# Kernel tuning notes

Hardware: AMD Instinct MI355X
Metric: run time of the kernel (lower is better)

## Reference

```python
import jax, jax.numpy as jnp
import numpy as np
from jax import lax

B, N, M = 4, 16384, 2048
C_IN = 64
RADII = (0.2, 0.4)
KS = (32, 64)
MLPS = ((64, 64, 128), (64, 96, 128))
EPS = 1e-5


def setup_inputs() -> dict:
    key = jax.random.key(0)
    ks = jax.random.split(key, 32)
    inp = {}
    inp["xyz"] = jax.random.uniform(ks[0], (B, 3, N), jnp.float32)
    inp["feature"] = jax.random.normal(ks[1], (B, C_IN, N), jnp.float32)
    ki = 2
    for s, chans in enumerate(MLPS):
        cin = C_IN + 3  # use_xyz concatenates relative xyz
        for l, cout in enumerate(chans):
            inp[f"w{s}{l}"] = jax.random.normal(ks[ki], (cout, cin), jnp.float32) * (1.0 / np.sqrt(cin)); ki += 1
            inp[f"g{s}{l}"] = jnp.ones((cout,), jnp.float32)
            inp[f"b{s}{l}"] = jnp.zeros((cout,), jnp.float32)
            cin = cout
    return inp


def _fps(points):
    """Farthest point sampling. points [N,3] -> [M] int32 indices (starts at 0)."""
    n = points.shape[0]
    def step(carry, _):
        dists, last = carry
        d = jnp.sum((points - points[last]) ** 2, axis=-1)
        dists = jnp.minimum(dists, d)
        nxt = jnp.argmax(dists).astype(jnp.int32)
        return (dists, nxt), nxt
    init = (jnp.full((n,), 1e10, jnp.float32), jnp.int32(0))
    _, rest = lax.scan(step, init, None, length=M - 1)
    return jnp.concatenate([jnp.zeros((1,), jnp.int32), rest])


def _ball_query(xyz, new_xyz, radius, k):
    """xyz [B,3,N], new_xyz [B,3,M] -> [B,M,k] int32. First-found semantics: empty
    slots are filled with the first valid index (pointnet2 ball_query behavior)."""
    xyz = lax.stop_gradient(xyz)
    new_xyz = lax.stop_gradient(new_xyz)
    n = xyz.shape[-1]
    sq_x = jnp.sum(xyz ** 2, axis=1)          # [B,N]
    sq_c = jnp.sum(new_xyz ** 2, axis=1)      # [B,M]
    d2 = sq_c[:, :, None] + sq_x[:, None, :] - 2.0 * jnp.einsum('bdm,bdn->bmn', new_xyz, xyz)
    scores = jnp.where(d2 < radius * radius, jnp.arange(n, dtype=jnp.int32), n)
    idx = -lax.top_k(-scores, k)[0]           # k smallest indices (in order)
    first = idx[..., :1]
    idx = jnp.where(idx >= n, first, idx)
    return jnp.where(idx >= n, 0, idx)


def _group(feat, idx):
    """feat [B,C,N], idx [B,M,K] -> [B,C,M,K]"""
    return jax.vmap(lambda f, i: f[:, i])(feat, idx)


def _forward(xyz, feature, params):
    idx = jax.vmap(_fps)(jnp.transpose(lax.stop_gradient(xyz), (0, 2, 1)))  # [B,M]
    new_xyz = jnp.take_along_axis(xyz, idx[:, None, :].astype(jnp.int32), axis=2)  # [B,3,M]
    feats = []
    for s in range(len(MLPS)):
        nidx = _ball_query(xyz, new_xyz, RADII[s], KS[s])        # [B,M,K]
        gxyz = _group(xyz, nidx) - new_xyz[..., None]            # [B,3,M,K]
        x = jnp.concatenate([gxyz, _group(feature, nidx)], axis=1)  # [B,3+C,M,K]
        for l in range(len(MLPS[s])):
            w = params[f"w{s}{l}"]; g = params[f"g{s}{l}"]; b = params[f"b{s}{l}"]
            x = jnp.einsum('oc,bcmk->bomk', w, x)                # 1x1 conv
            mu = jnp.mean(x, axis=(0, 2, 3), keepdims=True)      # train-mode BN
            var = jnp.mean((x - mu) ** 2, axis=(0, 2, 3), keepdims=True)
            x = (x - mu) * lax.rsqrt(var + EPS)
            x = x * g[None, :, None, None] + b[None, :, None, None]
            x = jax.nn.relu(x)
        feats.append(jnp.max(x, axis=3))                         # max over neighbors
    return new_xyz, jnp.concatenate(feats, axis=1)               # [B,3,M], [B,256,M]


def reference(xyz, feature, w00, g00, b00, w01, g01, b01, w02, g02, b02,
              w10, g10, b10, w11, g11, b11, w12, g12, b12):
    params = dict(w00=w00, g00=g00, b00=b00, w01=w01, g01=g01, b01=b01,
                  w02=w02, g02=g02, b02=b02, w10=w10, g10=g10, b10=b10,
                  w11=w11, g11=g11, b11=b11, w12=w12, g12=g12, b12=b12)
    return _forward(xyz, feature, params)
```

## Files before the change

### kernel.cpp

```cpp
#include <hip/hip_runtime.h>
#include <cstdint>

constexpr int B_ = 4, N_ = 16384, M_ = 2048;
constexpr int COLS0 = B_ * M_ * 32;
constexpr int COLS1 = B_ * M_ * 64;

constexpr size_t OFF_NEWXYZ = 0;
constexpr size_t OFF_NIDX0  = (size_t)B_ * 3 * M_ * 4;
constexpr size_t OFF_NIDX1  = OFF_NIDX0 + (size_t)COLS0 * 4;
constexpr size_t OFF_STATS  = OFF_NIDX1 + (size_t)COLS1 * 4;
constexpr size_t STATS_VALS = 64 * 2 * 128;
constexpr size_t OFF_COEF   = OFF_STATS + 6 * STATS_VALS * 8;
constexpr size_t OFF_MNMX   = OFF_COEF + 6 * 128 * 16;
constexpr size_t MNMX_ONE   = (size_t)B_ * M_ * 128 * 4;
constexpr size_t OFF_Z      = OFF_MNMX + 4 * MNMX_ONE;
constexpr int ZSTRIDE = 96 * 64;

__global__ __launch_bounds__(512, 2) void fps_kernel(const float* __restrict__ xyz,
                                                     float* __restrict__ newxyz,
                                                     float* __restrict__ outxyz) {
#pragma clang fp contract(off)
  int b = blockIdx.x, t = threadIdx.x;
  const float* xb = xyz + (size_t)b * 3 * N_;
  float px[32], py[32], pz[32], dd[32];
#pragma unroll
  for (int i = 0; i < 32; ++i) {
    int n = t + (i << 9);
    px[i] = xb[n]; py[i] = xb[N_ + n]; pz[i] = xb[2 * N_ + n];
    dd[i] = 1e10f;
    asm volatile("" : "+v"(px[i]), "+v"(py[i]), "+v"(pz[i]));
  }
  __shared__ float s_out[3 * M_];
  __shared__ unsigned long long s_red[8];
  __shared__ int s_w;
  float fx = xb[0], fy = xb[N_], fz = xb[2 * N_];
  if (t == 0) { s_out[0] = fx; s_out[M_] = fy; s_out[2 * M_] = fz; }
  int lane = t & 63, wid = t >> 6;
  for (int s = 1; s < M_; ++s) {
    float bv = -1.f; int bi = 0;
#pragma unroll
    for (int i = 0; i < 32; ++i) {
      float dx = px[i] - fx, dy = py[i] - fy, dz = pz[i] - fz;
      float d = (dx * dx + dy * dy) + dz * dz;
      float dm = dd[i];
      if (d < dm) dm = d;
      dd[i] = dm;
      if (dm > bv) { bv = dm; bi = t + (i << 9); }
    }
    unsigned long long key =
        ((unsigned long long)__float_as_uint(bv) << 32) | (unsigned)(0xFFFFFFFFu - (unsigned)bi);
#pragma unroll
    for (int off = 1; off < 64; off <<= 1) {
      unsigned long long o = __shfl_xor(key, off);
      if (o > key) key = o;
    }
    if (lane == 0) s_red[wid] = key;
    __syncthreads();
    if (wid == 0) {
      unsigned long long k2 = (lane < 8) ? s_red[lane] : 0ull;
#pragma unroll
      for (int off = 1; off < 8; off <<= 1) {
        unsigned long long o = __shfl_xor(k2, off);
        if (o > k2) k2 = o;
      }
      if (lane == 0) s_w = (int)(0xFFFFFFFFu - (unsigned)(k2 & 0xFFFFFFFFull));
    }
    __syncthreads();
    int w = s_w;
    fx = xb[w]; fy = xb[N_ + w]; fz = xb[2 * N_ + w];
    if (t == 0) { s_out[s] = fx; s_out[M_ + s] = fy; s_out[2 * M_ + s] = fz; }
  }
  __syncthreads();
  for (int e = t; e < 3 * M_; e += 512) {
    float v = s_out[e];
    newxyz[(size_t)b * 3 * M_ + e] = v;
    outxyz[(size_t)b * 3 * M_ + e] = v;
  }
}

template <int KNB>
__global__ __launch_bounds__(256) void bq_kernel(const float* __restrict__ xyz,
                                                 const float* __restrict__ newxyz,
                                                 int* __restrict__ nidx, float r2) {
#pragma clang fp contract(off)
  int t = threadIdx.x, lane = t & 63, wq = t >> 6;
  int q = blockIdx.x * 4 + wq;
  int b = q >> 11, m = q & 2047;
  const float* xb = xyz + (size_t)b * 3 * N_;
  float cx = newxyz[((size_t)b * 3 + 0) * M_ + m];
  float cy = newxyz[((size_t)b * 3 + 1) * M_ + m];
  float cz = newxyz[((size_t)b * 3 + 2) * M_ + m];
  float sqc = (cx * cx + cy * cy) + cz * cz;
  int found = 0, first = 0;
  for (int c = 0; c < N_ / 64; ++c) {
    int n = c * 64 + lane;
    float x = xb[n], y = xb[N_ + n], z = xb[2 * N_ + n];
    float sqx = (x * x + y * y) + z * z;
    float dot = fmaf(cz, z, fmaf(cy, y, cx * x));
    float d2 = (sqc + sqx) - 2.0f * dot;
    bool in = d2 < r2;
    unsigned long long mask = __ballot(in);
    if (mask) {
      if (found == 0) first = c * 64 + (__ffsll((long long)mask) - 1);
      int pos = found + __popcll(mask & ((1ull << lane) - 1ull));
      if (in && pos < KNB) nidx[(size_t)q * KNB + pos] = n;
      found += __popcll(mask);
      if (found >= KNB) break;
    }
  }
  if (found < KNB) {
    int fill = (found == 0) ? 0 : first;
    for (int s = found + lane; s < KNB; s += 64) nidx[(size_t)q * KNB + s] = fill;
  }
}

__device__ __forceinline__ void stat_accum(float acc, int o, int cout, double* stats,
                                           int part, int lane) {
  float v1 = acc, v2 = acc * acc;
#pragma unroll
  for (int off = 1; off < 64; off <<= 1) {
    v1 += __shfl_xor(v1, off);
    v2 += __shfl_xor(v2, off);
  }
  if (lane == 0) {
    atomicAdd(stats + ((size_t)part * 2 + 0) * cout + o, (double)v1);
    atomicAdd(stats + ((size_t)part * 2 + 1) * cout + o, (double)v2);
  }
}

template <int CIN, int G>
__device__ __forceinline__ void conv_sweep(const float* __restrict__ w, int o0,
                                           const float* sx, int lane, float* acc) {
  int o0u = __builtin_amdgcn_readfirstlane(o0);
  const float* wb = w + (size_t)o0u * CIN;
#pragma unroll
  for (int k = 0; k < G; ++k) acc[k] = 0.f;
#pragma unroll 8
  for (int c = 0; c < CIN; ++c) {
    float xv = sx[c * 64 + lane];
#pragma unroll
    for (int k = 0; k < G; ++k) acc[k] += wb[(size_t)(4 * k) * CIN + c] * xv;
  }
}

template <int CIN>
__device__ __forceinline__ void stage_bn(const float* __restrict__ zr,
                                         const float4* __restrict__ coefIn,
                                         float* sx, int t) {
  const float4* zr4 = (const float4*)zr;
  float4* sx4 = (float4*)sx;
  for (int e = t; e < CIN * 16; e += 256) {
    int c = e >> 4;
    float4 v = zr4[e];
    float4 cf = coefIn[c];
    float4 r;
    r.x = fmaxf(((v.x - cf.x) * cf.y) * cf.z + cf.w, 0.f);
    r.y = fmaxf(((v.y - cf.x) * cf.y) * cf.z + cf.w, 0.f);
    r.z = fmaxf(((v.z - cf.x) * cf.y) * cf.z + cf.w, 0.f);
    r.w = fmaxf(((v.w - cf.x) * cf.y) * cf.z + cf.w, 0.f);
    sx4[e] = r;
  }
}

template <int KNB>
__global__ __launch_bounds__(256) void convL0_kernel(
    const float* __restrict__ w0, const float* __restrict__ xyz,
    const float* __restrict__ feat, const int* __restrict__ nidx,
    const float* __restrict__ newxyz, float* __restrict__ Z, double* __restrict__ stats) {
  __shared__ float sx[67 * 64];
  __shared__ int snb[64];
  int rec = blockIdx.x, t = threadIdx.x, lane = t & 63, wid = t >> 6;
  if (t < 64) snb[t] = nidx[(size_t)rec * 64 + t];
  __syncthreads();
  for (int e = t; e < 67 * 64; e += 256) {
    int c = e >> 6, l = e & 63;
    int col = rec * 64 + l;
    int b = col / (M_ * KNB);
    int rem = col - b * (M_ * KNB);
    int m = rem / KNB;
    int n = snb[l];
    float v;
    if (c < 3) v = xyz[((size_t)b * 3 + c) * N_ + n] - newxyz[((size_t)b * 3 + c) * M_ + m];
    else       v = feat[((size_t)b * 64 + (c - 3)) * N_ + n];
    sx[e] = v;
  }
  __syncthreads();
  float* zr = Z + (size_t)rec * ZSTRIDE;
  int part = rec & 63;
  float acc[8];
#pragma unroll
  for (int g = 0; g < 2; ++g) {
    int o0 = wid + 32 * g;
    conv_sweep<67, 8>(w0, o0, sx, lane, acc);
#pragma unroll
    for (int k = 0; k < 8; ++k) {
      int o = o0 + 4 * k;
      zr[o * 64 + lane] = acc[k];
      stat_accum(acc[k], o, 64, stats, part, lane);
    }
  }
}

template <int CIN, int COUT>
__global__ __launch_bounds__(256) void convMid_kernel(
    const float* __restrict__ w, const float4* __restrict__ coefIn,
    float* __restrict__ Z, double* __restrict__ stats) {
  __shared__ float sx[CIN * 64];
  int rec = blockIdx.x, t = threadIdx.x, lane = t & 63, wid = t >> 6;
  float* zr = Z + (size_t)rec * ZSTRIDE;
  stage_bn<CIN>(zr, coefIn, sx, t);
  __syncthreads();
  int part = rec & 63;
  float acc[8];
#pragma unroll
  for (int g = 0; g < COUT / 32; ++g) {
    int o0 = wid + 32 * g;
    conv_sweep<CIN, 8>(w, o0, sx, lane, acc);
#pragma unroll
    for (int k = 0; k < 8; ++k) {
      int o = o0 + 4 * k;
      zr[o * 64 + lane] = acc[k];
      stat_accum(acc[k], o, COUT, stats, part, lane);
    }
  }
}

template <int CIN, int KNB>
__global__ __launch_bounds__(256) void convLast_kernel(
    const float* __restrict__ w, const float4* __restrict__ coefIn,
    const float* __restrict__ Z, double* __restrict__ stats,
    float* __restrict__ mx, float* __restrict__ mn) {
  __shared__ float sx[CIN * 64];
  int rec = blockIdx.x, t = threadIdx.x, lane = t & 63, wid = t >> 6;
  const float* zr = Z + (size_t)rec * ZSTRIDE;
  stage_bn<CIN>(zr, coefIn, sx, t);
  __syncthreads();
  int part = rec & 63;
  float acc[8];
#pragma unroll
  for (int g = 0; g < 4; ++g) {
    int o0 = wid + 32 * g;
    conv_sweep<CIN, 8>(w, o0, sx, lane, acc);
#pragma unroll
    for (int k = 0; k < 8; ++k) {
      int o = o0 + 4 * k;
      stat_accum(acc[k], o, 128, stats, part, lane);
      float vM = acc[k], vN = acc[k];
      if (KNB == 64) {
#pragma unroll
        for (int off = 1; off < 64; off <<= 1) {
          vM = fmaxf(vM, __shfl_xor(vM, off));
          vN = fminf(vN, __shfl_xor(vN, off));
        }
        if (lane == 0) {
          mx[(size_t)o * (B_ * M_) + rec] = vM;
          mn[(size_t)o * (B_ * M_) + rec] = vN;
        }
      } else {
#pragma unroll
        for (int off = 1; off < 32; off <<= 1) {
          vM = fmaxf(vM, __shfl_xor(vM, off));
          vN = fminf(vN, __shfl_xor(vN, off));
        }
        if ((lane & 31) == 0) {
          int grp = rec * 2 + (lane >> 5);
          mx[(size_t)o * (B_ * M_) + grp] = vM;
          mn[(size_t)o * (B_ * M_) + grp] = vN;
        }
      }
    }
  }
}

__global__ __launch_bounds__(256) void pool_fin_kernel(
    const float* __restrict__ mx, const float* __restrict__ mn,
    const float4* __restrict__ coefOut, float* __restrict__ outFeats, int chBase) {
  int idx = blockIdx.x * 256 + threadIdx.x;
  int o = idx >> 13;
  int gm = idx & 8191;
  float4 cf = coefOut[o];
  float vM = mx[idx], vN = mn[idx];
  float rM = ((vM - cf.x) * cf.y) * cf.z + cf.w;
  float rN = ((vN - cf.x) * cf.y) * cf.z + cf.w;
  float z = fmaxf(fmaxf(rM, rN), 0.f);
  int b = gm >> 11, m = gm & 2047;
  outFeats[((size_t)b * 256 + chBase + o) * M_ + m] = z;
}

__global__ void coef_kernel(const double* __restrict__ stats, const float* __restrict__ g,
                            const float* __restrict__ bb, float4* __restrict__ coef,
                            int cout, double invcnt) {
  int ch = threadIdx.x;
  if (ch >= cout) return;
  double s1 = 0.0, s2 = 0.0;
  for (int p = 0; p < 64; ++p) {
    s1 += stats[((size_t)p * 2 + 0) * cout + ch];
    s2 += stats[((size_t)p * 2 + 1) * cout + ch];
  }
  double mean = s1 * invcnt;
  double var = s2 * invcnt - mean * mean;
  double rstd = 1.0 / sqrt(var + 1e-5);
  coef[ch] = make_float4((float)mean, (float)rstd, g[ch], bb[ch]);
}

extern "C" void kernel_launch(void* const* d_in, const int* in_sizes, int n_in,
                              void* d_out, int out_size, void* d_ws, size_t ws_size,
                              hipStream_t stream) {
  const float* xyz  = (const float*)d_in[0];
  const float* feat = (const float*)d_in[1];
  const float* w00 = (const float*)d_in[2],  *g00 = (const float*)d_in[3],  *b00 = (const float*)d_in[4];
  const float* w01 = (const float*)d_in[5],  *g01 = (const float*)d_in[6],  *b01 = (const float*)d_in[7];
  const float* w02 = (const float*)d_in[8],  *g02 = (const float*)d_in[9],  *b02 = (const float*)d_in[10];
  const float* w10 = (const float*)d_in[11], *g10 = (const float*)d_in[12], *b10 = (const float*)d_in[13];
  const float* w11 = (const float*)d_in[14], *g11 = (const float*)d_in[15], *b11 = (const float*)d_in[16];
  const float* w12 = (const float*)d_in[17], *g12 = (const float*)d_in[18], *b12 = (const float*)d_in[19];

  char* ws = (char*)d_ws;
  float*  newxyz = (float*)(ws + OFF_NEWXYZ);
  int*    nidx0  = (int*)(ws + OFF_NIDX0);
  int*    nidx1  = (int*)(ws + OFF_NIDX1);
  double* stats  = (double*)(ws + OFF_STATS);
  float4* coef   = (float4*)(ws + OFF_COEF);
  float*  mx0    = (float*)(ws + OFF_MNMX + 0 * MNMX_ONE);
  float*  mn0    = (float*)(ws + OFF_MNMX + 1 * MNMX_ONE);
  float*  mx1    = (float*)(ws + OFF_MNMX + 2 * MNMX_ONE);
  float*  mn1    = (float*)(ws + OFF_MNMX + 3 * MNMX_ONE);
  float*  Z      = (float*)(ws + OFF_Z);
  float* outF = (float*)d_out;
  float* outFeats = outF + (size_t)B_ * 3 * M_;

  hipMemsetAsync(ws + OFF_STATS, 0, 6 * STATS_VALS * 8, stream);
  fps_kernel<<<B_, 512, 0, stream>>>(xyz, newxyz, outF);
  bq_kernel<32><<<(B_ * M_) / 4, 256, 0, stream>>>(xyz, newxyz, nidx0, (float)(0.2 * 0.2));
  bq_kernel<64><<<(B_ * M_) / 4, 256, 0, stream>>>(xyz, newxyz, nidx1, (float)(0.4 * 0.4));

  float4* c00 = coef + 0 * 128; float4* c01 = coef + 1 * 128; float4* c02 = coef + 2 * 128;
  float4* c10 = coef + 3 * 128; float4* c11 = coef + 4 * 128; float4* c12 = coef + 5 * 128;
  double* st0 = stats + 0 * STATS_VALS; double* st1 = stats + 1 * STATS_VALS;
  double* st2 = stats + 2 * STATS_VALS; double* st3 = stats + 3 * STATS_VALS;
  double* st4 = stats + 4 * STATS_VALS; double* st5 = stats + 5 * STATS_VALS;
  int gb0 = COLS0 / 64, gb1 = COLS1 / 64;
  int gfin = (128 * B_ * M_) / 256;

  convL0_kernel<32><<<gb0, 256, 0, stream>>>(w00, xyz, feat, nidx0, newxyz, Z, st0);
  coef_kernel<<<1, 128, 0, stream>>>(st0, g00, b00, c00, 64, 1.0 / COLS0);
  convMid_kernel<64, 64><<<gb0, 256, 0, stream>>>(w01, c00, Z, st1);
  coef_kernel<<<1, 128, 0, stream>>>(st1, g01, b01, c01, 64, 1.0 / COLS0);
  convLast_kernel<64, 32><<<gb0, 256, 0, stream>>>(w02, c01, Z, st2, mx0, mn0);
  coef_kernel<<<1, 128, 0, stream>>>(st2, g02, b02, c02, 128, 1.0 / COLS0);
  pool_fin_kernel<<<gfin, 256, 0, stream>>>(mx0, mn0, c02, outFeats, 0);

  convL0_kernel<64><<<gb1, 256, 0, stream>>>(w10, xyz, feat, nidx1, newxyz, Z, st3);
  coef_kernel<<<1, 128, 0, stream>>>(st3, g10, b10, c10, 64, 1.0 / COLS1);
  convMid_kernel<64, 96><<<gb1, 256, 0, stream>>>(w11, c10, Z, st4);
  coef_kernel<<<1, 128, 0, stream>>>(st4, g11, b11, c11, 96, 1.0 / COLS1);
  convLast_kernel<96, 64><<<gb1, 256, 0, stream>>>(w12, c11, Z, st5, mx1, mn1);
  coef_kernel<<<1, 128, 0, stream>>>(st5, g12, b12, c12, 128, 1.0 / COLS1);
  pool_fin_kernel<<<gfin, 256, 0, stream>>>(mx1, mn1, c12, outFeats, 128);
}
```

Before: 4.894 ms.

## Fuse FPS, ball query and first conv into persistent producer-consumer megakernel

Merges farthest point sampling, both ball queries and scale-1 layer-0 conv into one persistent kernel. Blocks take roles: 4 run FPS and publish centroids via atomics, 48 spin-wait on sentinel-initialized centroids to run ball queries, and the rest spin on neighbor indices to build the conv input and accumulate BN statistics. The goal is to hide the long serial FPS behind ball query and conv work instead of leaving the GPU mostly idle. It depends on all 256 blocks being co-resident and on sentinel memsets, and it adds atomic polling traffic. Scale-1 layers now run before scale-0.

```diff
diff --git a/kernel.cpp b/kernel.cpp
--- a/kernel.cpp
+++ b/kernel.cpp
@@ -16,80 +16,55 @@
 constexpr size_t OFF_Z      = OFF_MNMX + 4 * MNMX_ONE;
 constexpr int ZSTRIDE = 96 * 64;
 
-__global__ __launch_bounds__(512, 2) void fps_kernel(const float* __restrict__ xyz,
-                                                     float* __restrict__ newxyz,
-                                                     float* __restrict__ outxyz) {
+__device__ __forceinline__ void stat_accum(float acc, int o, int cout, double* stats,
+                                           int part, int lane) {
+  float v1 = acc, v2 = acc * acc;
+#pragma unroll
+  for (int off = 1; off < 64; off <<= 1) {
+    v1 += __shfl_xor(v1, off);
+    v2 += __shfl_xor(v2, off);
+  }
+  if (lane == 0) {
+    atomicAdd(stats + ((size_t)part * 2 + 0) * cout + o, (double)v1);
+    atomicAdd(stats + ((size_t)part * 2 + 1) * cout + o, (double)v2);
+  }
+}
+
+template <int CIN, int G>
+__device__ __forceinline__ void conv_sweep(const float* __restrict__ w, int o0,
+                                           const float* sx, int lane, float* acc) {
+  int o0u = __builtin_amdgcn_readfirstlane(o0);
+  const float* wb = w + (size_t)o0u * CIN;
+#pragma unroll
+  for (int k = 0; k < G; ++k) acc[k] = 0.f;
+#pragma unroll 8
+  for (int c = 0; c < CIN; ++c) {
+    float xv = sx[c * 64 + lane];
+#pragma unroll
+    for (int k = 0; k < G; ++k) acc[k] += wb[(size_t)(4 * k) * CIN + c] * xv;
+  }
+}
+
+template <int CIN>
+__device__ __forceinline__ void conv_sweep8(const float* __restrict__ w, int o0,
+                                            const float* sx, int lane, float* acc) {
+  int o0u = __builtin_amdgcn_readfirstlane(o0);
+  const float* wb = w + (size_t)o0u * CIN;
+#pragma unroll
+  for (int k = 0; k < 8; ++k) acc[k] = 0.f;
+#pragma unroll 8
+  for (int c = 0; c < CIN; ++c) {
+    float xv = sx[c * 64 + lane];
+#pragma unroll
+    for (int k = 0; k < 8; ++k) acc[k] += wb[(size_t)(8 * k) * CIN + c] * xv;
+  }
+}
+
+template <int KNB>
+__device__ void bq_wave(const float* __restrict__ xyz, int* __restrict__ nidx,
+                        int q, int b, float cx, float cy, float cz, float r2, int lane) {
 #pragma clang fp contract(off)
-  int b = blockIdx.x, t = threadIdx.x;
   const float* xb = xyz + (size_t)b * 3 * N_;
-  float px[32], py[32], pz[32], dd[32];
-#pragma unroll
-  for (int i = 0; i < 32; ++i) {
-    int n = t + (i << 9);
-    px[i] = xb[n]; py[i] = xb[N_ + n]; pz[i] = xb[2 * N_ + n];
-    dd[i] = 1e10f;
-    asm volatile("" : "+v"(px[i]), "+v"(py[i]), "+v"(pz[i]));
-  }
-  __shared__ float s_out[3 * M_];
-  __shared__ unsigned long long s_red[8];
-  __shared__ int s_w;
-  float fx = xb[0], fy = xb[N_], fz = xb[2 * N_];
-  if (t == 0) { s_out[0] = fx; s_out[M_] = fy; s_out[2 * M_] = fz; }
-  int lane = t & 63, wid = t >> 6;
-  for (int s = 1; s < M_; ++s) {
-    float bv = -1.f; int bi = 0;
-#pragma unroll
-    for (int i = 0; i < 32; ++i) {
-      float dx = px[i] - fx, dy = py[i] - fy, dz = pz[i] - fz;
-      float d = (dx * dx + dy * dy) + dz * dz;
-      float dm = dd[i];
-      if (d < dm) dm = d;
-      dd[i] = dm;
-      if (dm > bv) { bv = dm; bi = t + (i << 9); }
-    }
-    unsigned long long key =
-        ((unsigned long long)__float_as_uint(bv) << 32) | (unsigned)(0xFFFFFFFFu - (unsigned)bi);
-#pragma unroll
-    for (int off = 1; off < 64; off <<= 1) {
-      unsigned long long o = __shfl_xor(key, off);
-      if (o > key) key = o;
-    }
-    if (lane == 0) s_red[wid] = key;
-    __syncthreads();
-    if (wid == 0) {
-      unsigned long long k2 = (lane < 8) ? s_red[lane] : 0ull;
-#pragma unroll
-      for (int off = 1; off < 8; off <<= 1) {
-        unsigned long long o = __shfl_xor(k2, off);
-        if (o > k2) k2 = o;
-      }
-      if (lane == 0) s_w = (int)(0xFFFFFFFFu - (unsigned)(k2 & 0xFFFFFFFFull));
-    }
-    __syncthreads();
-    int w = s_w;
-    fx = xb[w]; fy = xb[N_ + w]; fz = xb[2 * N_ + w];
-    if (t == 0) { s_out[s] = fx; s_out[M_ + s] = fy; s_out[2 * M_ + s] = fz; }
-  }
-  __syncthreads();
-  for (int e = t; e < 3 * M_; e += 512) {
-    float v = s_out[e];
-    newxyz[(size_t)b * 3 * M_ + e] = v;
-    outxyz[(size_t)b * 3 * M_ + e] = v;
-  }
-}
-
-template <int KNB>
-__global__ __launch_bounds__(256) void bq_kernel(const float* __restrict__ xyz,
-                                                 const float* __restrict__ newxyz,
-                                                 int* __restrict__ nidx, float r2) {
-#pragma clang fp contract(off)
-  int t = threadIdx.x, lane = t & 63, wq = t >> 6;
-  int q = blockIdx.x * 4 + wq;
-  int b = q >> 11, m = q & 2047;
-  const float* xb = xyz + (size_t)b * 3 * N_;
-  float cx = newxyz[((size_t)b * 3 + 0) * M_ + m];
-  float cy = newxyz[((size_t)b * 3 + 1) * M_ + m];
-  float cz = newxyz[((size_t)b * 3 + 2) * M_ + m];
   float sqc = (cx * cx + cy * cy) + cz * cz;
   int found = 0, first = 0;
   for (int c = 0; c < N_ / 64; ++c) {
@@ -103,43 +78,150 @@
     if (mask) {
       if (found == 0) first = c * 64 + (__ffsll((long long)mask) - 1);
       int pos = found + __popcll(mask & ((1ull << lane) - 1ull));
-      if (in && pos < KNB) nidx[(size_t)q * KNB + pos] = n;
+      if (in && pos < KNB) atomicExch(&nidx[(size_t)q * KNB + pos], n);
       found += __popcll(mask);
       if (found >= KNB) break;
     }
   }
   if (found < KNB) {
     int fill = (found == 0) ? 0 : first;
-    for (int s = found + lane; s < KNB; s += 64) nidx[(size_t)q * KNB + s] = fill;
-  }
-}
-
-__device__ __forceinline__ void stat_accum(float acc, int o, int cout, double* stats,
-                                           int part, int lane) {
-  float v1 = acc, v2 = acc * acc;
-#pragma unroll
-  for (int off = 1; off < 64; off <<= 1) {
-    v1 += __shfl_xor(v1, off);
-    v2 += __shfl_xor(v2, off);
-  }
-  if (lane == 0) {
-    atomicAdd(stats + ((size_t)part * 2 + 0) * cout + o, (double)v1);
-    atomicAdd(stats + ((size_t)part * 2 + 1) * cout + o, (double)v2);
-  }
-}
-
-template <int CIN, int G>
-__device__ __forceinline__ void conv_sweep(const float* __restrict__ w, int o0,
-                                           const float* sx, int lane, float* acc) {
-  int o0u = __builtin_amdgcn_readfirstlane(o0);
-  const float* wb = w + (size_t)o0u * CIN;
-#pragma unroll
-  for (int k = 0; k < G; ++k) acc[k] = 0.f;
-#pragma unroll 8
-  for (int c = 0; c < CIN; ++c) {
-    float xv = sx[c * 64 + lane];
-#pragma unroll
-    for (int k = 0; k < G; ++k) acc[k] += wb[(size_t)(4 * k) * CIN + c] * xv;
+    for (int s2 = found + lane; s2 < KNB; s2 += 64) atomicExch(&nidx[(size_t)q * KNB + s2], fill);
+  }
+}
+
+__global__ __launch_bounds__(512, 2) void mega_kernel(
+    const float* __restrict__ xyz, const float* __restrict__ feat,
+    float* __restrict__ newxyz, float* __restrict__ outxyz,
+    int* __restrict__ nidx0, int* __restrict__ nidx1,
+    float* __restrict__ Z, double* __restrict__ st3, const float* __restrict__ w10) {
+  __shared__ __align__(16) char smem[98304];
+  int bid = blockIdx.x, t = threadIdx.x, lane = t & 63, wid = t >> 6;
+
+  if (bid < 4) {
+#pragma clang fp contract(off)
+    float* s_out = (float*)smem;
+    unsigned long long* s_red = (unsigned long long*)(smem + 24576);
+    int* s_w = (int*)(smem + 24640);
+    int b = bid;
+    const float* xb = xyz + (size_t)b * 3 * N_;
+    float px[32], py[32], pz[32], dd[32];
+#pragma unroll
+    for (int i = 0; i < 32; ++i) {
+      int n = t + (i << 9);
+      px[i] = xb[n]; py[i] = xb[N_ + n]; pz[i] = xb[2 * N_ + n];
+      dd[i] = 1e10f;
+      asm volatile("" : "+v"(px[i]), "+v"(py[i]), "+v"(pz[i]));
+    }
+    size_t base = (size_t)b * 3 * M_;
+    float fx = xb[0], fy = xb[N_], fz = xb[2 * N_];
+    if (t == 0) {
+      s_out[0] = fx; s_out[M_] = fy; s_out[2 * M_] = fz;
+      atomicExch(&newxyz[base], fx); atomicExch(&newxyz[base + M_], fy);
+      atomicExch(&newxyz[base + 2 * M_], fz);
+    }
+    for (int s = 1; s < M_; ++s) {
+      float bv = -1.f; int bi = 0;
+#pragma unroll
+      for (int i = 0; i < 32; ++i) {
+        float dx = px[i] - fx, dy = py[i] - fy, dz = pz[i] - fz;
+        float d = (dx * dx + dy * dy) + dz * dz;
+        float dm = dd[i];
+        if (d < dm) dm = d;
+        dd[i] = dm;
+        if (dm > bv) { bv = dm; bi = t + (i << 9); }
+      }
+      unsigned long long key =
+          ((unsigned long long)__float_as_uint(bv) << 32) | (unsigned)(0xFFFFFFFFu - (unsigned)bi);
+#pragma unroll
+      for (int off = 1; off < 64; off <<= 1) {
+        unsigned long long o = __shfl_xor(key, off);
+        if (o > key) key = o;
+      }
+      if (lane == 0) s_red[wid] = key;
+      __syncthreads();
+      if (wid == 0) {
+        unsigned long long k2 = (lane < 8) ? s_red[lane] : 0ull;
+#pragma unroll
+        for (int off = 1; off < 8; off <<= 1) {
+          unsigned long long o = __shfl_xor(k2, off);
+          if (o > k2) k2 = o;
+        }
+        if (lane == 0) *s_w = (int)(0xFFFFFFFFu - (unsigned)(k2 & 0xFFFFFFFFull));
+      }
+      __syncthreads();
+      int w = *s_w;
+      fx = xb[w]; fy = xb[N_ + w]; fz = xb[2 * N_ + w];
+      if (t == 0) {
+        s_out[s] = fx; s_out[M_ + s] = fy; s_out[2 * M_ + s] = fz;
+        atomicExch(&newxyz[base + s], fx); atomicExch(&newxyz[base + M_ + s], fy);
+        atomicExch(&newxyz[base + 2 * M_ + s], fz);
+      }
+    }
+    __syncthreads();
+    for (int e = t; e < 3 * M_; e += 512) outxyz[base + e] = s_out[e];
+  } else if (bid < 52) {
+    int waveId = (bid - 4) * 8 + wid;
+    for (int T = waveId; T < 2 * B_ * M_; T += 48 * 8) {
+      int mg = T >> 1;
+      int b = mg >> 11, m = mg & 2047;
+      unsigned vv = 0;
+      if (lane < 3) {
+        unsigned* p = (unsigned*)(newxyz + ((size_t)b * 3 + lane) * M_ + m);
+        for (int it = 0; it < (1 << 18); ++it) {
+          vv = atomicAdd(p, 0u);
+          if (vv != 0xFFFFFFFFu) break;
+          __builtin_amdgcn_s_sleep(16);
+        }
+      }
+      float cx = __uint_as_float(__shfl((int)vv, 0));
+      float cy = __uint_as_float(__shfl((int)vv, 1));
+      float cz = __uint_as_float(__shfl((int)vv, 2));
+      if (T & 1) bq_wave<64>(xyz, nidx1, mg, b, cx, cy, cz, (float)(0.4 * 0.4), lane);
+      else       bq_wave<32>(xyz, nidx0, mg, b, cx, cy, cz, (float)(0.2 * 0.2), lane);
+    }
+  } else {
+    float* sx   = (float*)smem;
+    int*   snb  = (int*)(smem + 17152);
+    float* sctr = (float*)(smem + 17152 + 256);
+    for (int R = bid - 52; R < COLS1 / 64; R += 204) {
+      __syncthreads();
+      if (wid == 0) {
+        int* p = nidx1 + (size_t)R * 64 + lane;
+        int v = -1;
+        for (int it = 0; it < (1 << 18); ++it) {
+          v = atomicAdd(p, 0);
+          if (v != -1) break;
+          __builtin_amdgcn_s_sleep(64);
+        }
+        snb[lane] = (v < 0) ? 0 : v;
+        if (lane < 3) {
+          int b = R >> 11, m = R & 2047;
+          sctr[lane] = __uint_as_float(
+              atomicAdd((unsigned*)(newxyz + ((size_t)b * 3 + lane) * M_ + m), 0u));
+        }
+      }
+      __syncthreads();
+      int b = R >> 11;
+      for (int e = t; e < 67 * 64; e += 512) {
+        int c = e >> 6, l = e & 63;
+        int n = snb[l];
+        float v;
+        if (c < 3) v = xyz[((size_t)b * 3 + c) * N_ + n] - sctr[c];
+        else       v = feat[((size_t)b * 64 + (c - 3)) * N_ + n];
+        sx[e] = v;
+      }
+      __syncthreads();
+      float* zr = Z + (size_t)R * ZSTRIDE;
+      int part = R & 63;
+      float acc[8];
+      conv_sweep8<67>(w10, wid, sx, lane, acc);
+#pragma unroll
+      for (int k = 0; k < 8; ++k) {
+        int o = wid + 8 * k;
+        zr[o * 64 + lane] = acc[k];
+        stat_accum(acc[k], o, 64, st3, part, lane);
+      }
+    }
   }
 }
 
@@ -329,11 +411,6 @@
   float* outF = (float*)d_out;
   float* outFeats = outF + (size_t)B_ * 3 * M_;
 
-  hipMemsetAsync(ws + OFF_STATS, 0, 6 * STATS_VALS * 8, stream);
-  fps_kernel<<<B_, 512, 0, stream>>>(xyz, newxyz, outF);
-  bq_kernel<32><<<(B_ * M_) / 4, 256, 0, stream>>>(xyz, newxyz, nidx0, (float)(0.2 * 0.2));
-  bq_kernel<64><<<(B_ * M_) / 4, 256, 0, stream>>>(xyz, newxyz, nidx1, (float)(0.4 * 0.4));
-
   float4* c00 = coef + 0 * 128; float4* c01 = coef + 1 * 128; float4* c02 = coef + 2 * 128;
   float4* c10 = coef + 3 * 128; float4* c11 = coef + 4 * 128; float4* c12 = coef + 5 * 128;
   double* st0 = stats + 0 * STATS_VALS; double* st1 = stats + 1 * STATS_VALS;
@@ -342,6 +419,19 @@
   int gb0 = COLS0 / 64, gb1 = COLS1 / 64;
   int gfin = (128 * B_ * M_) / 256;
 
+  hipMemsetAsync(ws + OFF_STATS, 0, 6 * STATS_VALS * 8, stream);
+  hipMemsetAsync(newxyz, 0xFF, (size_t)B_ * 3 * M_ * 4, stream);
+  hipMemsetAsync(nidx1, 0xFF, (size_t)COLS1 * 4, stream);
+
+  mega_kernel<<<256, 512, 0, stream>>>(xyz, feat, newxyz, outF, nidx0, nidx1, Z, st3, w10);
+
+  coef_kernel<<<1, 128, 0, stream>>>(st3, g10, b10, c10, 64, 1.0 / COLS1);
+  convMid_kernel<64, 96><<<gb1, 256, 0, stream>>>(w11, c10, Z, st4);
+  coef_kernel<<<1, 128, 0, stream>>>(st4, g11, b11, c11, 96, 1.0 / COLS1);
+  convLast_kernel<96, 64><<<gb1, 256, 0, stream>>>(w12, c11, Z, st5, mx1, mn1);
+  coef_kernel<<<1, 128, 0, stream>>>(st5, g12, b12, c12, 128, 1.0 / COLS1);
+  pool_fin_kernel<<<gfin, 256, 0, stream>>>(mx1, mn1, c12, outFeats, 128);
+
   convL0_kernel<32><<<gb0, 256, 0, stream>>>(w00, xyz, feat, nidx0, newxyz, Z, st0);
   coef_kernel<<<1, 128, 0, stream>>>(st0, g00, b00, c00, 64, 1.0 / COLS0);
   convMid_kernel<64, 64><<<gb0, 256, 0, stream>>>(w01, c00, Z, st1);
@@ -349,12 +439,4 @@
   convLast_kernel<64, 32><<<gb0, 256, 0, stream>>>(w02, c01, Z, st2, mx0, mn0);
   coef_kernel<<<1, 128, 0, stream>>>(st2, g02, b02, c02, 128, 1.0 / COLS0);
   pool_fin_kernel<<<gfin, 256, 0, stream>>>(mx0, mn0, c02, outFeats, 0);
-
-  convL0_kernel<64><<<gb1, 256, 0, stream>>>(w10, xyz, feat, nidx1, newxyz, Z, st3);
-  coef_kernel<<<1, 128, 0, stream>>>(st3, g10, b10, c10, 64, 1.0 / COLS1);
-  convMid_kernel<64, 96><<<gb1, 256, 0, stream>>>(w11, c10, Z, st4);
-  coef_kernel<<<1, 128, 0, stream>>>(st4, g11, b11, c11, 96, 1.0 / COLS1);
-  convLast_kernel<96, 64><<<gb1, 256, 0, stream>>>(w12, c11, Z, st5, mx1, mn1);
-  coef_kernel<<<1, 128, 0, stream>>>(st5, g12, b12, c12, 128, 1.0 / COLS1);
-  pool_fin_kernel<<<gfin, 256, 0, stream>>>(mx1, mn1, c12, outFeats, 128);
-}
+}
```

New measurement: 4.999 ms. 2.1% more time.
